# Kernel tuning notes

Measured on AMD Instinct MI355X. Metric: run time of the kernel, lower is better.

## Reference

```python
import jax, jax.numpy as jnp
import numpy as np

N = 50000   # nodes
E = 800000  # edges
D = 128     # input_size == hidden_size
R = 4       # n_relations
L = 3       # n_layers


def setup_inputs() -> dict:
    key = jax.random.key(0)
    ks = jax.random.split(key, 8)
    x = jax.random.normal(ks[0], (N, D), dtype=jnp.float32)
    edge_index = jax.random.randint(ks[1], (2, E), 0, N, dtype=jnp.int32)
    edge_type = jax.random.randint(ks[2], (E,), 0, R, dtype=jnp.int32)
    scale = 1.0 / np.sqrt(D)
    W = jax.random.normal(ks[3], (L, R, D, D), dtype=jnp.float32) * scale      # per-relation weights
    root = jax.random.normal(ks[4], (L, D, D), dtype=jnp.float32) * scale      # root (self) weights
    bias = jnp.zeros((L, D), dtype=jnp.float32)
    gamma = jnp.ones((L, D), dtype=jnp.float32)   # LayerNorm weight
    beta = jnp.zeros((L, D), dtype=jnp.float32)   # LayerNorm bias
    return {"x": x, "edge_index": edge_index, "edge_type": edge_type,
            "W": W, "root": root, "bias": bias, "gamma": gamma, "beta": beta}


def _rgcn_conv(x, src, dst, etype, W_r, W_root, b):
    # Transform all nodes by every relation weight once: [R, N, D]
    h = jnp.einsum('ni,rio->rno', x, W_r)
    msg = h[etype, src]                                   # [E, D] per-edge messages
    # mean aggregation per (dst, relation), matching PyG RGCNConv aggr='mean'
    seg = dst * R + etype                                 # combined segment id
    cnt = jax.ops.segment_sum(jnp.ones((E,), x.dtype), seg, num_segments=N * R)
    inv = 1.0 / jnp.maximum(cnt, 1.0)
    agg = jax.ops.segment_sum(msg * inv[seg][:, None], dst, num_segments=N)
    return agg + x @ W_root + b


def _layernorm(x, g, b, eps=1e-5):
    mu = jnp.mean(x, axis=-1, keepdims=True)
    var = jnp.var(x, axis=-1, keepdims=True)
    return (x - mu) * jax.lax.rsqrt(var + eps) * g + b


def reference(x, edge_index, edge_type, W, root, bias, gamma, beta):
    src, dst = edge_index[0], edge_index[1]
    for i in range(L):
        x_res = x
        x = _rgcn_conv(x, src, dst, edge_type, W[i], root[i], bias[i])
        x = jax.nn.relu(x)
        # dropout p=0.0 -> no-op; residual_projection is Identity (input_size==hidden_size)
        x = x + x_res
        x = _layernorm(x, gamma[i], beta[i])
    return x
```

## Files before the change

kernel.cpp:

```cpp
#include <hip/hip_runtime.h>
#include <stdint.h>

#define NN 50000
#define EE 800000
#define DD 128
#define RR 4
#define LL 3
#define NRSEG (NN*RR)
#define NKB 20
#define NB_SCAN ((NRSEG + 1023)/1024)
#define NBK NB_SCAN
#define BKCAP 5120
#define WCONV_T (LL*NKB*8*64)

typedef _Float16 f16;
typedef _Float16 f16x8 __attribute__((ext_vector_type(8)));
typedef float f32x4 __attribute__((ext_vector_type(4)));

union U32H { uint32_t u; f16 h[2]; };
union U4H  { uint4 u; f16 h[8]; };

__global__ __launch_bounds__(1024) void k_binA(const int* __restrict__ ei, const int* __restrict__ et,
                                               int* __restrict__ cnt, int* __restrict__ bcur,
                                               uint2* __restrict__ tmp){
  __shared__ int bcnt[NBK];
  __shared__ int bbase[NBK];
  int t = threadIdx.x;
  if(t < NBK) bcnt[t] = 0;
  __syncthreads();

  int seg[4], src[4], bk[4], rk[4];
  #pragma unroll
  for(int j=0;j<4;j++){
    int e = blockIdx.x*4096 + j*1024 + t;
    if(e < EE){
      src[j] = ei[e];
      seg[j] = ei[EE+e]*RR + et[e];
      bk[j]  = seg[j] >> 10;
      rk[j]  = atomicAdd(&bcnt[bk[j]], 1);
      atomicAdd(&cnt[seg[j]], 1);
    } else { seg[j] = -1; }
  }
  __syncthreads();
  if(t < NBK){
    int c = bcnt[t];
    bbase[t] = (c > 0) ? atomicAdd(&bcur[t], c) : 0;
  }
  __syncthreads();
  #pragma unroll
  for(int j=0;j<4;j++){
    if(seg[j] >= 0){
      uint2 p; p.x = (uint32_t)seg[j]; p.y = (uint32_t)src[j];
      tmp[(size_t)bk[j]*BKCAP + bbase[bk[j]] + rk[j]] = p;
    }
  }
}

__global__ __launch_bounds__(256) void k_reduce(const int* __restrict__ cnt, int* __restrict__ bsum){
  __shared__ int s[256];
  int b = blockIdx.x, t = threadIdx.x;
  int base = b*1024 + t*4;
  int v = 0;
  #pragma unroll
  for(int j=0;j<4;j++){ int i = base+j; if(i<NRSEG) v += cnt[i]; }
  s[t]=v; __syncthreads();
  for(int o=128;o>0;o>>=1){ if(t<o) s[t]+=s[t+o]; __syncthreads(); }
  if(t==0) bsum[b]=s[0];
}

__global__ __launch_bounds__(256) void k_top(const int* __restrict__ bsum, int* __restrict__ boff,
                                             int* __restrict__ rowp, int nb){
  __shared__ int s[256];
  int t=threadIdx.x;
  int v = (t<nb)? bsum[t] : 0;
  s[t]=v; __syncthreads();
  for(int o=1;o<256;o<<=1){ int x=(t>=o)?s[t-o]:0; __syncthreads(); s[t]+=x; __syncthreads(); }
  if(t<nb) boff[t] = s[t]-v;
  if(t==255) rowp[NRSEG] = s[255];
}

__global__ __launch_bounds__(256) void k_scan(const int* __restrict__ cnt, const int* __restrict__ boff,
                                              int* __restrict__ rowp){
  __shared__ int s[256];
  int b=blockIdx.x, t=threadIdx.x;
  int base = b*1024 + t*4;
  int c[4]; int tot=0;
  #pragma unroll
  for(int j=0;j<4;j++){ int i=base+j; c[j] = (i<NRSEG)? cnt[i]:0; tot+=c[j]; }
  s[t]=tot; __syncthreads();
  for(int o=1;o<256;o<<=1){ int x=(t>=o)?s[t-o]:0; __syncthreads(); s[t]+=x; __syncthreads(); }
  int run = boff[b] + s[t]-tot;
  #pragma unroll
  for(int j=0;j<4;j++){
    int i=base+j;
    if(i<NRSEG){ rowp[i]=run; run+=c[j]; }
  }
}

__global__ __launch_bounds__(512) void k_binB(const int* __restrict__ rowp, const int* __restrict__ bcur,
                                              const uint2* __restrict__ tmp, int* __restrict__ ssrc){
  __shared__ int lcur[1024];
  int b = blockIdx.x, t = threadIdx.x;
  lcur[t] = 0; lcur[t+512] = 0;
  __syncthreads();
  int n = bcur[b];
  const uint2* src = tmp + (size_t)b*BKCAP;
  for(int i = t; i < n; i += 512){
    uint2 p = src[i];
    int pos = rowp[p.x] + atomicAdd(&lcur[p.x & 1023], 1);
    ssrc[pos] = (int)p.y;
  }
}

__global__ __launch_bounds__(256) void k_convWX(const float* __restrict__ W, const float* __restrict__ root,
                                                f16* __restrict__ Wf,
                                                const float* __restrict__ x, f16* __restrict__ x16){
  int t = blockIdx.x*256 + threadIdx.x;
  if(t < WCONV_T){
    int lane = t & 63;
    int cb   = (t>>6) & 7;
    int kb   = (t>>9) % NKB;
    int l    = (t>>9) / NKB;
    int col  = cb*16 + (lane&15);
    int kbase= kb*32 + (lane>>4)*8;
    f16* dst = Wf + (size_t)t*8;
    #pragma unroll
    for(int e=0;e<8;e++){
      int k = kbase+e;
      float v = (k < 4*DD) ? W[(((size_t)l*RR + (k>>7))*DD + (k&127))*DD + col]
                           : root[((size_t)l*DD + (k-4*DD))*DD + col];
      dst[e] = (f16)v;
    }
  } else {
    int u = t - WCONV_T;
    if(u < NN*DD/8){
      const float4* xf = (const float4*)x + (size_t)u*2;
      float4 a = xf[0], b = xf[1];
      U4H o;
      o.h[0]=(f16)a.x; o.h[1]=(f16)a.y; o.h[2]=(f16)a.z; o.h[3]=(f16)a.w;
      o.h[4]=(f16)b.x; o.h[5]=(f16)b.y; o.h[6]=(f16)b.z; o.h[7]=(f16)b.w;
      ((uint4*)x16)[u] = o.u;
    }
  }
}

__device__ __forceinline__ void acc8(float a[8], uint4 v){
  U4H w; w.u = v;
  #pragma unroll
  for(int k=0;k<8;k++) a[k] += (float)w.h[k];
}

__global__ __launch_bounds__(256) void k_agg(const f16* __restrict__ x16, const int* __restrict__ rowp,
                                             const int* __restrict__ ssrc, f16* __restrict__ A16){
  int seg = blockIdx.x*16 + (threadIdx.x >> 4);
  int l   = threadIdx.x & 15;
  if(seg >= NRSEG) return;

  int b = rowp[seg], e = rowp[seg+1];
  int n = e - b;
  const uint4* xl = (const uint4*)x16 + l;

  float acc[8];
  #pragma unroll
  for(int k=0;k<8;k++) acc[k] = 0.f;

  for(int base=0; base<n; base+=4){
    int m = n - base;
    int i0 = b + base;
    int c0 = ssrc[i0];
    int c1 = (m>1) ? ssrc[i0+1] : c0;
    int c2 = (m>2) ? ssrc[i0+2] : c0;
    int c3 = (m>3) ? ssrc[i0+3] : c0;
    uint4 v0 = xl[(size_t)c0*16];
    uint4 v1 = xl[(size_t)c1*16];
    uint4 v2 = xl[(size_t)c2*16];
    uint4 v3 = xl[(size_t)c3*16];
    acc8(acc, v0);
    if(m>1) acc8(acc, v1);
    if(m>2) acc8(acc, v2);
    if(m>3) acc8(acc, v3);
  }

  float inv = 1.f/(float)max(n,1);
  U4H o;
  #pragma unroll
  for(int k=0;k<8;k++) o.h[k] = (f16)(acc[k]*inv);
  ((uint4*)A16)[(size_t)seg*16 + l] = o.u;
}

__device__ __forceinline__ void stageB(const f16* __restrict__ Wf, f16* lds, int kb, int wid, int lane){
  const f16* src = Wf + (size_t)kb*4096;
  #pragma unroll
  for(int j=wid;j<8;j+=4){
    __builtin_amdgcn_global_load_lds((const __attribute__((address_space(1))) void*)(src + j*512 + lane*8),
                                     (__attribute__((address_space(3))) void*)(lds + j*512), 16, 0, 0);
  }
}

template<int LAST>
__global__ __launch_bounds__(256) void k_gemm(const f16* __restrict__ A16, const f16* __restrict__ x16,
                                              const f16* __restrict__ Wf,
                                              const float* __restrict__ bias, const float* __restrict__ gmm,
                                              const float* __restrict__ bet,
                                              f16* __restrict__ xnext, float* __restrict__ outf){
  __shared__ f16 Blds[2][4096];
  int tid  = threadIdx.x;
  int lane = tid & 63, wid = tid >> 6;
  int rbase = blockIdx.x*128 + wid*32;
  int fr = lane & 15, kg = lane >> 4;

  int arow0 = rbase + fr;       if(arow0 >= NN) arow0 = NN-1;
  int arow1 = rbase + 16 + fr;  if(arow1 >= NN) arow1 = NN-1;
  const f16* Ar0 = A16 + (size_t)arow0*512 + kg*8;
  const f16* Ar1 = A16 + (size_t)arow1*512 + kg*8;
  const f16* Xr0 = x16 + (size_t)arow0*128 + kg*8;
  const f16* Xr1 = x16 + (size_t)arow1*128 + kg*8;

  f32x4 acc[2][8];
  #pragma unroll
  for(int r=0;r<2;r++)
    #pragma unroll
    for(int c=0;c<8;c++) acc[r][c] = (f32x4){0.f,0.f,0.f,0.f};

  f16x8 a0, a1;
  a0 = *(const f16x8*)(Ar0); a1 = *(const f16x8*)(Ar1);
  stageB(Wf, &Blds[0][0], 0, wid, lane);

  for(int kb=0; kb<NKB; kb++){
    __syncthreads();
    if(kb+1 < NKB) stageB(Wf, &Blds[(kb+1)&1][0], kb+1, wid, lane);
    f16x8 na0 = a0, na1 = a1;
    if(kb+1 < NKB){
      if(kb+1 < 16){ na0 = *(const f16x8*)(Ar0 + (kb+1)*32); na1 = *(const f16x8*)(Ar1 + (kb+1)*32); }
      else         { na0 = *(const f16x8*)(Xr0 + (kb+1-16)*32); na1 = *(const f16x8*)(Xr1 + (kb+1-16)*32); }
    }
    const f16* bb = &Blds[kb&1][lane*8];
    #pragma unroll
    for(int cb=0;cb<8;cb++){
      f16x8 b = *(const f16x8*)(bb + cb*512);
      acc[0][cb] = __builtin_amdgcn_mfma_f32_16x16x32_f16(a0, b, acc[0][cb], 0, 0, 0);
      acc[1][cb] = __builtin_amdgcn_mfma_f32_16x16x32_f16(a1, b, acc[1][cb], 0, 0, 0);
    }
    a0 = na0; a1 = na1;
  }

  float bs[8];
  #pragma unroll
  for(int cb=0;cb<8;cb++) bs[cb] = bias[cb*16 + fr];
  int g4 = kg*4;
  #pragma unroll
  for(int rh=0; rh<2; rh++){
    float vv[8][4];
    #pragma unroll
    for(int cb=0;cb<8;cb++){
      int col = cb*16 + fr;
      #pragma unroll
      for(int q=0;q<4;q++){
        float v = acc[rh][cb][q] + bs[cb];
        v = v > 0.f ? v : 0.f;
        int row = rbase + rh*16 + g4 + q;
        float res = (row < NN) ? (float)x16[(size_t)row*128 + col] : 0.f;
        vv[cb][q] = v + res;
      }
    }
    #pragma unroll
    for(int q=0;q<4;q++){
      float s1=0.f, s2=0.f;
      #pragma unroll
      for(int cb=0;cb<8;cb++){ float v=vv[cb][q]; s1+=v; s2+=v*v; }
      #pragma unroll
      for(int m=1;m<16;m<<=1){ s1 += __shfl_xor(s1,m,16); s2 += __shfl_xor(s2,m,16); }
      float mu  = s1*(1.f/128.f);
      float var = s2*(1.f/128.f) - mu*mu;
      float rs  = rsqrtf(var + 1e-5f);
      int row = rbase + rh*16 + g4 + q;
      if(row < NN){
        #pragma unroll
        for(int cb=0;cb<8;cb++){
          int col = cb*16 + fr;
          float y = (vv[cb][q]-mu)*rs*gmm[col] + bet[col];
          if(LAST) outf[(size_t)row*128 + col] = y;
          else     xnext[(size_t)row*128 + col] = (f16)y;
        }
      }
    }
  }
}

extern "C" void kernel_launch(void* const* d_in, const int* in_sizes, int n_in,
                              void* d_out, int out_size, void* d_ws, size_t ws_size,
                              hipStream_t stream){
  const float* x    = (const float*)d_in[0];
  const int*   ei   = (const int*)d_in[1];
  const int*   et   = (const int*)d_in[2];
  const float* W    = (const float*)d_in[3];
  const float* root = (const float*)d_in[4];
  const float* bias = (const float*)d_in[5];
  const float* gmm  = (const float*)d_in[6];
  const float* bet  = (const float*)d_in[7];

  char* ws = (char*)d_ws;
  int*   cnt  = (int*)(ws + 0);
  int*   bcur = (int*)(ws + 800000);
  int*   rowp = (int*)(ws + 801792);
  int*   bsum = (int*)(ws + 1602048);
  int*   boff = (int*)(ws + 1603072);
  int*   ssrc = (int*)(ws + 1604096);
  f16*   Wf   = (f16*)(ws + 4804608);
  f16*   x16a = (f16*)(ws + 5296128);
  f16*   x16b = (f16*)(ws + 18096128);
  f16*   A16  = (f16*)(ws + 30896128);
  uint2* tmp  = (uint2*)A16;

  hipMemsetAsync(cnt, 0, 800784, stream);
  k_binA  <<<NBK, 1024, 0, stream>>>(ei, et, cnt, bcur, tmp);
  k_reduce<<<NB_SCAN, 256, 0, stream>>>(cnt, bsum);
  k_top   <<<1, 256, 0, stream>>>(bsum, boff, rowp, NB_SCAN);
  k_scan  <<<NB_SCAN, 256, 0, stream>>>(cnt, boff, rowp);
  k_binB  <<<NBK, 512, 0, stream>>>(rowp, bcur, tmp, ssrc);
  k_convWX<<<(WCONV_T + NN*DD/8 + 255)/256, 256, 0, stream>>>(W, root, Wf, x, x16a);

  f16* xc = x16a; f16* xn = x16b;
  for(int l=0; l<LL; l++){
    k_agg<<<NRSEG/16, 256, 0, stream>>>(xc, rowp, ssrc, A16);
    if(l < LL-1)
      k_gemm<0><<<(NN+127)/128, 256, 0, stream>>>(A16, xc, Wf + (size_t)l*81920,
                                                  bias+l*DD, gmm+l*DD, bet+l*DD, xn, nullptr);
    else
      k_gemm<1><<<(NN+127)/128, 256, 0, stream>>>(A16, xc, Wf + (size_t)l*81920,
                                                  bias+l*DD, gmm+l*DD, bet+l*DD, nullptr, (float*)d_out);
    f16* t = xc; xc = xn; xn = t;
  }
}
```

Baseline: 261.2 us.

## Fuse CSR scan stages using bucket counts and widen binning grids

Removes the separate block-reduce and top-level scan kernels. Each scan block now derives its global offset directly from the per-bucket edge totals (bcur) that k_binA already accumulated, since buckets coincide with scan blocks of 1024 segments. k_binA is launched with one edge per thread across about 782 blocks instead of four edges per thread across 196, and k_binB uses 1024 threads. This cuts two launches and raises parallelism in the preprocessing phase, at the cost of more global atomics on bcur and a redundant small reduction in every scan block.

New measurement: 266.6 us. 2.0% more time.

```diff
diff --git a/kernel.cpp b/kernel.cpp
--- a/kernel.cpp
+++ b/kernel.cpp
@@ -29,17 +29,14 @@
   if(t < NBK) bcnt[t] = 0;
   __syncthreads();
 
-  int seg[4], src[4], bk[4], rk[4];
-  #pragma unroll
-  for(int j=0;j<4;j++){
-    int e = blockIdx.x*4096 + j*1024 + t;
-    if(e < EE){
-      src[j] = ei[e];
-      seg[j] = ei[EE+e]*RR + et[e];
-      bk[j]  = seg[j] >> 10;
-      rk[j]  = atomicAdd(&bcnt[bk[j]], 1);
-      atomicAdd(&cnt[seg[j]], 1);
-    } else { seg[j] = -1; }
+  int e = blockIdx.x*1024 + t;
+  int seg = -1, src = 0, bk = 0, rk = 0;
+  if(e < EE){
+    src = ei[e];
+    seg = ei[EE+e]*RR + et[e];
+    bk  = seg >> 10;
+    rk  = atomicAdd(&bcnt[bk], 1);
+    atomicAdd(&cnt[seg], 1);
   }
   __syncthreads();
   if(t < NBK){
@@ -47,49 +44,39 @@
     bbase[t] = (c > 0) ? atomicAdd(&bcur[t], c) : 0;
   }
   __syncthreads();
-  #pragma unroll
-  for(int j=0;j<4;j++){
-    if(seg[j] >= 0){
-      uint2 p; p.x = (uint32_t)seg[j]; p.y = (uint32_t)src[j];
-      tmp[(size_t)bk[j]*BKCAP + bbase[bk[j]] + rk[j]] = p;
-    }
-  }
-}
-
-__global__ __launch_bounds__(256) void k_reduce(const int* __restrict__ cnt, int* __restrict__ bsum){
+  if(seg >= 0){
+    uint2 p; p.x = (uint32_t)seg; p.y = (uint32_t)src;
+    tmp[(size_t)bk*BKCAP + bbase[bk] + rk] = p;
+  }
+}
+
+__global__ __launch_bounds__(256) void k_scan(const int* __restrict__ cnt, const int* __restrict__ bcur,
+                                              int* __restrict__ rowp){
   __shared__ int s[256];
   int b = blockIdx.x, t = threadIdx.x;
-  int base = b*1024 + t*4;
-  int v = 0;
-  #pragma unroll
-  for(int j=0;j<4;j++){ int i = base+j; if(i<NRSEG) v += cnt[i]; }
-  s[t]=v; __syncthreads();
+
+  int v = (t < NBK) ? bcur[t] : 0;
+  s[t] = (t < b) ? v : 0;
+  __syncthreads();
   for(int o=128;o>0;o>>=1){ if(t<o) s[t]+=s[t+o]; __syncthreads(); }
-  if(t==0) bsum[b]=s[0];
-}
-
-__global__ __launch_bounds__(256) void k_top(const int* __restrict__ bsum, int* __restrict__ boff,
-                                             int* __restrict__ rowp, int nb){
-  __shared__ int s[256];
-  int t=threadIdx.x;
-  int v = (t<nb)? bsum[t] : 0;
-  s[t]=v; __syncthreads();
-  for(int o=1;o<256;o<<=1){ int x=(t>=o)?s[t-o]:0; __syncthreads(); s[t]+=x; __syncthreads(); }
-  if(t<nb) boff[t] = s[t]-v;
-  if(t==255) rowp[NRSEG] = s[255];
-}
-
-__global__ __launch_bounds__(256) void k_scan(const int* __restrict__ cnt, const int* __restrict__ boff,
-                                              int* __restrict__ rowp){
-  __shared__ int s[256];
-  int b=blockIdx.x, t=threadIdx.x;
+  int boff_b = s[0];
+  __syncthreads();
+
+  if(b == NBK-1){
+    s[t] = v;
+    __syncthreads();
+    for(int o=128;o>0;o>>=1){ if(t<o) s[t]+=s[t+o]; __syncthreads(); }
+    if(t==0) rowp[NRSEG] = s[0];
+    __syncthreads();
+  }
+
   int base = b*1024 + t*4;
   int c[4]; int tot=0;
   #pragma unroll
   for(int j=0;j<4;j++){ int i=base+j; c[j] = (i<NRSEG)? cnt[i]:0; tot+=c[j]; }
   s[t]=tot; __syncthreads();
   for(int o=1;o<256;o<<=1){ int x=(t>=o)?s[t-o]:0; __syncthreads(); s[t]+=x; __syncthreads(); }
-  int run = boff[b] + s[t]-tot;
+  int run = boff_b + s[t]-tot;
   #pragma unroll
   for(int j=0;j<4;j++){
     int i=base+j;
@@ -97,15 +84,15 @@
   }
 }
 
-__global__ __launch_bounds__(512) void k_binB(const int* __restrict__ rowp, const int* __restrict__ bcur,
-                                              const uint2* __restrict__ tmp, int* __restrict__ ssrc){
+__global__ __launch_bounds__(1024) void k_binB(const int* __restrict__ rowp, const int* __restrict__ bcur,
+                                               const uint2* __restrict__ tmp, int* __restrict__ ssrc){
   __shared__ int lcur[1024];
   int b = blockIdx.x, t = threadIdx.x;
-  lcur[t] = 0; lcur[t+512] = 0;
+  lcur[t] = 0;
   __syncthreads();
   int n = bcur[b];
   const uint2* src = tmp + (size_t)b*BKCAP;
-  for(int i = t; i < n; i += 512){
+  for(int i = t; i < n; i += 1024){
     uint2 p = src[i];
     int pos = rowp[p.x] + atomicAdd(&lcur[p.x & 1023], 1);
     ssrc[pos] = (int)p.y;
@@ -303,8 +290,6 @@
   int*   cnt  = (int*)(ws + 0);
   int*   bcur = (int*)(ws + 800000);
   int*   rowp = (int*)(ws + 801792);
-  int*   bsum = (int*)(ws + 1602048);
-  int*   boff = (int*)(ws + 1603072);
   int*   ssrc = (int*)(ws + 1604096);
   f16*   Wf   = (f16*)(ws + 4804608);
   f16*   x16a = (f16*)(ws + 5296128);
@@ -313,11 +298,9 @@
   uint2* tmp  = (uint2*)A16;
 
   hipMemsetAsync(cnt, 0, 800784, stream);
-  k_binA  <<<NBK, 1024, 0, stream>>>(ei, et, cnt, bcur, tmp);
-  k_reduce<<<NB_SCAN, 256, 0, stream>>>(cnt, bsum);
-  k_top   <<<1, 256, 0, stream>>>(bsum, boff, rowp, NB_SCAN);
-  k_scan  <<<NB_SCAN, 256, 0, stream>>>(cnt, boff, rowp);
-  k_binB  <<<NBK, 512, 0, stream>>>(rowp, bcur, tmp, ssrc);
+  k_binA  <<<(EE+1023)/1024, 1024, 0, stream>>>(ei, et, cnt, bcur, tmp);
+  k_scan  <<<NB_SCAN, 256, 0, stream>>>(cnt, bcur, rowp);
+  k_binB  <<<NBK, 1024, 0, stream>>>(rowp, bcur, tmp, ssrc);
   k_convWX<<<(WCONV_T + NN*DD/8 + 255)/256, 256, 0, stream>>>(W, root, Wf, x, x16a);
 
   f16* xc = x16a; f16* xn = x16b;
```
